# Kernel optimization log

Measured on AMD Instinct MI355X. Metric: run time of the kernel, lower is better.

## Reference

```python
import jax, jax.numpy as jnp
import numpy as np

N, H, E, G, OUT = 50000, 128, 600000, 256, 64
NUM_ITERS = 5
GAMMA = 0.1
EPS = 0.1
NEG_SLOPE = 0.01


def setup_inputs() -> dict:
    key = jax.random.key(0)
    ks = jax.random.split(key, 10)
    s = 1.0 / np.sqrt(H)
    x = jax.random.normal(ks[0], (N, H), dtype=jnp.float32)
    edge_index = jax.random.randint(ks[1], (2, E), 0, N, dtype=jnp.int64)
    batch = jnp.sort(jax.random.randint(ks[2], (N,), 0, G, dtype=jnp.int64))
    W = jax.random.normal(ks[3], (H, H), dtype=jnp.float32) * s
    bias = jax.random.normal(ks[4], (H,), dtype=jnp.float32) * s
    lin_w = jax.random.normal(ks[5], (H, H), dtype=jnp.float32) * s
    l1_w = jax.random.normal(ks[6], (3 * H // 2, 3 * H), dtype=jnp.float32) / np.sqrt(3 * H)
    l1_b = jax.random.normal(ks[7], (3 * H // 2,), dtype=jnp.float32) * 0.01
    l2_w = jax.random.normal(ks[8], (OUT, 3 * H // 2), dtype=jnp.float32) / np.sqrt(3 * H // 2)
    l2_b = jax.random.normal(ks[9], (OUT,), dtype=jnp.float32) * 0.01
    return {"x": x, "edge_index": edge_index, "batch": batch, "W": W, "bias": bias,
            "lin_w": lin_w, "l1_w": l1_w, "l1_b": l1_b, "l2_w": l2_w, "l2_b": l2_b}


def reference(x, edge_index, batch, W, bias, lin_w, l1_w, l1_b, l2_w, l2_b):
    n = x.shape[0]
    src, dst = edge_index[0], edge_index[1]
    # antisymmetric weight: W - W^T - gamma*I
    A = W - W.T - GAMMA * jnp.eye(W.shape[0], dtype=x.dtype)
    for _ in range(NUM_ITERS):
        neigh = x @ lin_w.T                                   # [N,H] linear (no bias)
        agg = jax.ops.segment_sum(neigh[src], dst, num_segments=n)  # gather-scatter add
        conv = x @ A.T + agg + bias
        x = x + EPS * jnp.tanh(conv)
    # triple global pooling per graph: add / max / mean
    add = jax.ops.segment_sum(x, batch, num_segments=G)
    mx = jax.ops.segment_max(x, batch, num_segments=G)
    cnt = jax.ops.segment_sum(jnp.ones((n,), dtype=x.dtype), batch, num_segments=G)
    safe_cnt = jnp.maximum(cnt, 1.0)[:, None]
    mean = add / safe_cnt
    mx = jnp.where(cnt[:, None] > 0, mx, 0.0)
    pooled = jnp.concatenate([add, mx, mean], axis=1)          # [G, 3H]
    h = jax.nn.leaky_relu(pooled @ l1_w.T + l1_b, NEG_SLOPE)
    out = jax.nn.leaky_relu(h @ l2_w.T + l2_b, NEG_SLOPE)
    return out
```

## Files before the change

kernel.cpp:

```cpp
#include <hip/hip_runtime.h>
#include <hip/hip_fp16.h>
#include <cmath>

#define H 128
#define GAMMA 0.1f
#define EPS 0.1f
#define NEG 0.01f
#define NGRAPH 256

typedef _Float16 half_t;
typedef _Float16 f16x8 __attribute__((ext_vector_type(8)));
typedef _Float16 f16x4 __attribute__((ext_vector_type(4)));
typedef _Float16 f16x2 __attribute__((ext_vector_type(2)));
typedef float f32x4 __attribute__((ext_vector_type(4)));

__device__ __forceinline__ float fast_tanh(float v) {
    float e = __builtin_amdgcn_exp2f(v * 2.8853900817779268f);
    float r = __builtin_amdgcn_rcpf(e + 1.0f);
    return 1.0f - 2.0f * r;
}

__global__ __launch_bounds__(256) void prep_cast_zero(
        const float* __restrict__ W, const float* __restrict__ lin_w,
        half_t* __restrict__ WtTf, const float* __restrict__ x,
        half_t* __restrict__ xh, int n4, int* __restrict__ deg, int N) {
    int stride = gridDim.x * 256;
    int tot = max(n4, max(32768, N));
    for (int i = blockIdx.x * 256 + threadIdx.x; i < tot; i += stride) {
        if (i < n4) {
            float4 v = *(const float4*)(x + (size_t)i * 4);
            half_t* o = xh + (size_t)i * 4;
            o[0] = (half_t)v.x; o[1] = (half_t)v.y; o[2] = (half_t)v.z; o[3] = (half_t)v.w;
        }
        if (i < 32768) {
            int t = i & 7;
            int lane = (i >> 3) & 63;
            int ct = (i >> 9) & 7;
            int s = i >> 12;
            int q = lane >> 4, m = lane & 15;
            int j = ct * 16 + m;
            int k = s * 32 + q * 8 + t;
            float v;
            if (k < H) v = W[j * H + k] - W[k * H + j] - (j == k ? GAMMA : 0.f);
            else       v = lin_w[j * H + (k - H)];
            WtTf[i] = (half_t)v;
        }
        if (i < N) deg[i] = 0;
    }
}

__global__ __launch_bounds__(256) void count_kernel(const int* __restrict__ dst,
                                                    int* __restrict__ deg, int E) {
    int stride = gridDim.x * 256;
    for (int e = blockIdx.x * 256 + threadIdx.x; e < E; e += stride)
        atomicAdd(&deg[dst[e]], 1);
}

#define SCHUNK 2048
__global__ __launch_bounds__(256) void scan_part(const int* __restrict__ deg,
                                                 int* __restrict__ partials, int N) {
    __shared__ int red[256];
    int t = threadIdx.x, b = blockIdx.x;
    int base = b * SCHUNK + t * 8;
    int s = 0;
#pragma unroll
    for (int i = 0; i < 8; ++i) { int idx = base + i; if (idx < N) s += deg[idx]; }
    red[t] = s;
    __syncthreads();
    for (int off = 128; off > 0; off >>= 1) {
        if (t < off) red[t] += red[t + off];
        __syncthreads();
    }
    if (t == 0) partials[b] = red[0];
}

__global__ void scan_mid(const int* __restrict__ partials, int* __restrict__ blkoff, int nblk) {
    int lane = threadIdx.x;
    int p = (lane < nblk) ? partials[lane] : 0;
    int v = p;
    for (int off = 1; off < 64; off <<= 1) {
        int u = __shfl_up(v, off);
        if (lane >= off) v += u;
    }
    if (lane < nblk) blkoff[lane] = v - p;
}

__global__ __launch_bounds__(256) void scan_final(const int* __restrict__ deg,
        const int* __restrict__ blkoff, int* __restrict__ row_start,
        int* __restrict__ cursor, int N, int E) {
    __shared__ int red[256];
    int t = threadIdx.x, b = blockIdx.x;
    int base = b * SCHUNK + t * 8;
    int v[8]; int s = 0;
#pragma unroll
    for (int i = 0; i < 8; ++i) { int idx = base + i; v[i] = (idx < N) ? deg[idx] : 0; s += v[i]; }
    red[t] = s;
    __syncthreads();
    for (int off = 1; off < 256; off <<= 1) {
        int u = (t >= off) ? red[t - off] : 0;
        __syncthreads();
        red[t] += u;
        __syncthreads();
    }
    int run = blkoff[b] + red[t] - s;
#pragma unroll
    for (int i = 0; i < 8; ++i) {
        int idx = base + i;
        if (idx < N) { row_start[idx] = run; cursor[idx] = run; run += v[i]; }
    }
    if (b == 0 && t == 0) row_start[N] = E;
}

__global__ __launch_bounds__(256) void fill_kernel(const int* __restrict__ src,
        const int* __restrict__ dst, int* __restrict__ cursor,
        int* __restrict__ csr_src, int E) {
    int stride = gridDim.x * 256;
    for (int e = blockIdx.x * 256 + threadIdx.x; e < E; e += stride) {
        int p = atomicAdd(&cursor[dst[e]], 1);
        csr_src[p] = src[e];
    }
}

__global__ __launch_bounds__(256) void gather_agg(const half_t* __restrict__ xh,
        const int* __restrict__ row_start, const int* __restrict__ csr_src,
        half_t* __restrict__ xaggh, int N) {
    int wid = __builtin_amdgcn_readfirstlane(blockIdx.x * 4 + (threadIdx.x >> 6));
    int nwaves = gridDim.x * 4;
    int lane = threadIdx.x & 63;
    for (int node = wid; node < N; node += nwaves) {
        int begin = row_start[node];
        int end   = row_start[node + 1];
        f16x2 accA = (f16x2){(half_t)0.f, (half_t)0.f};
        f16x2 accB = (f16x2){(half_t)0.f, (half_t)0.f};
        for (int base = begin; base < end; base += 64) {
            int cnt = min(64, end - base);
            int myidx = csr_src[base + min(lane, cnt - 1)];
            int j = 0;
            for (; j + 7 < cnt; j += 8) {
                int s0 = __builtin_amdgcn_readlane(myidx, j + 0);
                int s1 = __builtin_amdgcn_readlane(myidx, j + 1);
                int s2 = __builtin_amdgcn_readlane(myidx, j + 2);
                int s3 = __builtin_amdgcn_readlane(myidx, j + 3);
                int s4 = __builtin_amdgcn_readlane(myidx, j + 4);
                int s5 = __builtin_amdgcn_readlane(myidx, j + 5);
                int s6 = __builtin_amdgcn_readlane(myidx, j + 6);
                int s7 = __builtin_amdgcn_readlane(myidx, j + 7);
                f16x2 v0 = *(const f16x2*)(xh + (size_t)s0 * H + lane * 2);
                f16x2 v1 = *(const f16x2*)(xh + (size_t)s1 * H + lane * 2);
                f16x2 v2 = *(const f16x2*)(xh + (size_t)s2 * H + lane * 2);
                f16x2 v3 = *(const f16x2*)(xh + (size_t)s3 * H + lane * 2);
                f16x2 v4 = *(const f16x2*)(xh + (size_t)s4 * H + lane * 2);
                f16x2 v5 = *(const f16x2*)(xh + (size_t)s5 * H + lane * 2);
                f16x2 v6 = *(const f16x2*)(xh + (size_t)s6 * H + lane * 2);
                f16x2 v7 = *(const f16x2*)(xh + (size_t)s7 * H + lane * 2);
                accA += v0; accB += v1; accA += v2; accB += v3;
                accA += v4; accB += v5; accA += v6; accB += v7;
            }
            if (cnt - j >= 4) {
                int s0 = __builtin_amdgcn_readlane(myidx, j + 0);
                int s1 = __builtin_amdgcn_readlane(myidx, j + 1);
                int s2 = __builtin_amdgcn_readlane(myidx, j + 2);
                int s3 = __builtin_amdgcn_readlane(myidx, j + 3);
                f16x2 v0 = *(const f16x2*)(xh + (size_t)s0 * H + lane * 2);
                f16x2 v1 = *(const f16x2*)(xh + (size_t)s1 * H + lane * 2);
                f16x2 v2 = *(const f16x2*)(xh + (size_t)s2 * H + lane * 2);
                f16x2 v3 = *(const f16x2*)(xh + (size_t)s3 * H + lane * 2);
                accA += v0; accB += v1; accA += v2; accB += v3;
                j += 4;
            }
            int rem = cnt - j;
            if (rem > 0) {
                int s0 = __builtin_amdgcn_readlane(myidx, j);
                int s1 = __builtin_amdgcn_readlane(myidx, min(j + 1, cnt - 1));
                int s2 = __builtin_amdgcn_readlane(myidx, min(j + 2, cnt - 1));
                f16x2 v0 = *(const f16x2*)(xh + (size_t)s0 * H + lane * 2);
                f16x2 v1 = *(const f16x2*)(xh + (size_t)s1 * H + lane * 2);
                f16x2 v2 = *(const f16x2*)(xh + (size_t)s2 * H + lane * 2);
                accA += v0;
                if (rem > 1) accB += v1;
                if (rem > 2) accA += v2;
            }
        }
        f16x2 o = accA + accB;
        *(f16x2*)(xaggh + (size_t)node * H + lane * 2) = o;
    }
}

#define CROWS 128
__global__ __launch_bounds__(256) void conv_mfma(
        const half_t* __restrict__ xh, const half_t* __restrict__ xaggh,
        const half_t* __restrict__ WtTf, const float* __restrict__ bias,
        half_t* __restrict__ xhout, int N) {
    int tid = threadIdx.x;
    int wave = tid >> 6, lane = tid & 63;
    int q = lane >> 4, m = lane & 15;
    int n0 = blockIdx.x * CROWS + wave * 32;

    f32x4 acc[2][8];
#pragma unroll
    for (int rt = 0; rt < 2; ++rt)
#pragma unroll
        for (int ct = 0; ct < 8; ++ct) acc[rt][ct] = (f32x4){0.f, 0.f, 0.f, 0.f};

#pragma unroll
    for (int s = 0; s < 8; ++s) {
        f16x8 afrag[2];
#pragma unroll
        for (int rt = 0; rt < 2; ++rt) {
            int row = min(n0 + rt * 16 + m, N - 1);
            afrag[rt] = (s < 4)
                ? *(const f16x8*)(xh    + (size_t)row * H + s * 32 + q * 8)
                : *(const f16x8*)(xaggh + (size_t)row * H + (s - 4) * 32 + q * 8);
        }
#pragma unroll
        for (int ct = 0; ct < 8; ++ct) {
            f16x8 bfrag = *(const f16x8*)(WtTf + ((s * 8 + ct) * 64 + lane) * 8);
            acc[0][ct] = __builtin_amdgcn_mfma_f32_16x16x32_f16(afrag[0], bfrag, acc[0][ct], 0, 0, 0);
            acc[1][ct] = __builtin_amdgcn_mfma_f32_16x16x32_f16(afrag[1], bfrag, acc[1][ct], 0, 0, 0);
        }
    }

#pragma unroll
    for (int rt = 0; rt < 2; ++rt) {
#pragma unroll
        for (int r = 0; r < 4; ++r) {
            int row = n0 + rt * 16 + q * 4 + r;
            if (row < N) {
#pragma unroll
                for (int ct = 0; ct < 8; ++ct) {
                    int col = ct * 16 + m;
                    float c = acc[rt][ct][r] + bias[col];
                    float o = (float)xh[(size_t)row * H + col] + EPS * fast_tanh(c);
                    xhout[(size_t)row * H + col] = (half_t)o;
                }
            }
        }
    }
}

__global__ __launch_bounds__(1024) void pool_mlp(const half_t* __restrict__ x,
        const int* __restrict__ batch,
        const float* __restrict__ l1_w, const float* __restrict__ l1_b,
        const float* __restrict__ l2_w, const float* __restrict__ l2_b,
        float* __restrict__ out, int N) {
    __shared__ float ssum[8][128];
    __shared__ float smax[8][128];
    __shared__ __align__(16) float sp[384];
    __shared__ __align__(16) float sh[192];
    int g = blockIdx.x, t = threadIdx.x;
    int feat = t & 127, slot = t >> 7;
    int lo = 0, hi = N;
    while (lo < hi) { int mid = (lo + hi) >> 1; if (batch[mid] < g) lo = mid + 1; else hi = mid; }
    int start = lo;
    hi = N;
    while (lo < hi) { int mid = (lo + hi) >> 1; if (batch[mid] < g + 1) lo = mid + 1; else hi = mid; }
    int end = lo;
    float sum = 0.f, mx = -INFINITY;
    for (int n = start + slot; n < end; n += 8) {
        float v = (float)x[(size_t)n * H + feat];
        sum += v;
        mx = fmaxf(mx, v);
    }
    ssum[slot][feat] = sum;
    smax[slot][feat] = mx;
    __syncthreads();
    if (t < 128) {
        float s = 0.f, m = -INFINITY;
#pragma unroll
        for (int k = 0; k < 8; ++k) { s += ssum[k][t]; m = fmaxf(m, smax[k][t]); }
        int cnt = end - start;
        sp[t] = s;
        sp[128 + t] = (cnt > 0) ? m : 0.f;
        sp[256 + t] = s / (float)(cnt > 0 ? cnt : 1);
    }
    __syncthreads();
    if (t < 192) {
        float acc = l1_b[t];
        const float* wr = l1_w + (size_t)t * 384;
        for (int k = 0; k < 384; k += 4) {
            float4 w = *(const float4*)(wr + k);
            float4 p = *(const float4*)(sp + k);
            acc += w.x * p.x + w.y * p.y + w.z * p.z + w.w * p.w;
        }
        sh[t] = acc > 0.f ? acc : NEG * acc;
    }
    __syncthreads();
    if (t < 64) {
        float acc = l2_b[t];
        const float* wr = l2_w + (size_t)t * 192;
        for (int k = 0; k < 192; k += 4) {
            float4 w = *(const float4*)(wr + k);
            float4 p = *(const float4*)(sh + k);
            acc += w.x * p.x + w.y * p.y + w.z * p.z + w.w * p.w;
        }
        out[g * 64 + t] = acc > 0.f ? acc : NEG * acc;
    }
}

extern "C" void kernel_launch(void* const* d_in, const int* in_sizes, int n_in,
                              void* d_out, int out_size, void* d_ws, size_t ws_size,
                              hipStream_t stream) {
    const float* x0    = (const float*)d_in[0];
    const int*   edge  = (const int*)d_in[1];
    const int*   batch = (const int*)d_in[2];
    const float* W     = (const float*)d_in[3];
    const float* bias  = (const float*)d_in[4];
    const float* lin_w = (const float*)d_in[5];
    const float* l1_w  = (const float*)d_in[6];
    const float* l1_b  = (const float*)d_in[7];
    const float* l2_w  = (const float*)d_in[8];
    const float* l2_b  = (const float*)d_in[9];
    float* out = (float*)d_out;

    int N = in_sizes[0] / H;
    int E = in_sizes[1] / 2;
    const int* src = edge;
    const int* dst = edge + E;

    size_t nh = (size_t)N * H;
    half_t* xhA    = (half_t*)d_ws;
    half_t* xhB    = xhA + nh;
    half_t* xaggh  = xhB + nh;
    half_t* WtTf   = xaggh + nh;
    int* deg       = (int*)(WtTf + 32768);
    int* row_start = deg + N;
    int* cursor    = row_start + N + 1;
    int* csr_src   = cursor + N;
    int* partials  = csr_src + E;
    int* blkoff    = partials + 64;

    int n4 = (int)(nh / 4);
    prep_cast_zero<<<1024, 256, 0, stream>>>(W, lin_w, WtTf, x0, xhA, n4, deg, N);

    count_kernel<<<1024, 256, 0, stream>>>(dst, deg, E);
    int nblk = (N + SCHUNK - 1) / SCHUNK;
    scan_part<<<nblk, 256, 0, stream>>>(deg, partials, N);
    scan_mid<<<1, 64, 0, stream>>>(partials, blkoff, nblk);
    scan_final<<<nblk, 256, 0, stream>>>(deg, blkoff, row_start, cursor, N, E);
    fill_kernel<<<1024, 256, 0, stream>>>(src, dst, cursor, csr_src, E);

    const half_t* xcur_h = xhA;
    int nblocks = (N + CROWS - 1) / CROWS;
    for (int it = 0; it < 5; ++it) {
        gather_agg<<<2048, 256, 0, stream>>>(xcur_h, row_start, csr_src, xaggh, N);
        half_t* xnext_h = (it & 1) ? xhA : xhB;
        conv_mfma<<<nblocks, 256, 0, stream>>>(xcur_h, xaggh, WtTf, bias, xnext_h, N);
        xcur_h = xnext_h;
    }

    pool_mlp<<<NGRAPH, 1024, 0, stream>>>(xcur_h, batch, l1_w, l1_b, l2_w, l2_b, out, N);
}
```

Measured before the change: 381.2 us.

## Permute weight columns for vectorized conv epilogue and halve rows per wave

```diff
diff --git a/kernel.cpp b/kernel.cpp
--- a/kernel.cpp
+++ b/kernel.cpp
@@ -38,7 +38,7 @@
             int ct = (i >> 9) & 7;
             int s = i >> 12;
             int q = lane >> 4, m = lane & 15;
-            int j = ct * 16 + m;
+            int j = m * 8 + ct;
             int k = s * 32 + q * 8 + t;
             float v;
             if (k < H) v = W[j * H + k] - W[k * H + j] - (j == k ? GAMMA : 0.f);
@@ -186,7 +186,7 @@
     }
 }
 
-#define CROWS 128
+#define CROWS 64
 __global__ __launch_bounds__(256) void conv_mfma(
         const half_t* __restrict__ xh, const half_t* __restrict__ xaggh,
         const half_t* __restrict__ WtTf, const float* __restrict__ bias,
@@ -194,46 +194,40 @@
     int tid = threadIdx.x;
     int wave = tid >> 6, lane = tid & 63;
     int q = lane >> 4, m = lane & 15;
-    int n0 = blockIdx.x * CROWS + wave * 32;
-
-    f32x4 acc[2][8];
-#pragma unroll
-    for (int rt = 0; rt < 2; ++rt)
-#pragma unroll
-        for (int ct = 0; ct < 8; ++ct) acc[rt][ct] = (f32x4){0.f, 0.f, 0.f, 0.f};
-
+    int n0 = blockIdx.x * CROWS + wave * 16;
+
+    f32x4 acc[8];
+#pragma unroll
+    for (int ct = 0; ct < 8; ++ct) acc[ct] = (f32x4){0.f, 0.f, 0.f, 0.f};
+
+    int arow = min(n0 + m, N - 1);
 #pragma unroll
     for (int s = 0; s < 8; ++s) {
-        f16x8 afrag[2];
-#pragma unroll
-        for (int rt = 0; rt < 2; ++rt) {
-            int row = min(n0 + rt * 16 + m, N - 1);
-            afrag[rt] = (s < 4)
-                ? *(const f16x8*)(xh    + (size_t)row * H + s * 32 + q * 8)
-                : *(const f16x8*)(xaggh + (size_t)row * H + (s - 4) * 32 + q * 8);
-        }
+        f16x8 afrag = (s < 4)
+            ? *(const f16x8*)(xh    + (size_t)arow * H + s * 32 + q * 8)
+            : *(const f16x8*)(xaggh + (size_t)arow * H + (s - 4) * 32 + q * 8);
 #pragma unroll
         for (int ct = 0; ct < 8; ++ct) {
             f16x8 bfrag = *(const f16x8*)(WtTf + ((s * 8 + ct) * 64 + lane) * 8);
-            acc[0][ct] = __builtin_amdgcn_mfma_f32_16x16x32_f16(afrag[0], bfrag, acc[0][ct], 0, 0, 0);
-            acc[1][ct] = __builtin_amdgcn_mfma_f32_16x16x32_f16(afrag[1], bfrag, acc[1][ct], 0, 0, 0);
-        }
-    }
-
-#pragma unroll
-    for (int rt = 0; rt < 2; ++rt) {
-#pragma unroll
-        for (int r = 0; r < 4; ++r) {
-            int row = n0 + rt * 16 + q * 4 + r;
-            if (row < N) {
-#pragma unroll
-                for (int ct = 0; ct < 8; ++ct) {
-                    int col = ct * 16 + m;
-                    float c = acc[rt][ct][r] + bias[col];
-                    float o = (float)xh[(size_t)row * H + col] + EPS * fast_tanh(c);
-                    xhout[(size_t)row * H + col] = (half_t)o;
-                }
+            acc[ct] = __builtin_amdgcn_mfma_f32_16x16x32_f16(afrag, bfrag, acc[ct], 0, 0, 0);
+        }
+    }
+
+    float4 b0 = *(const float4*)(bias + m * 8);
+    float4 b1 = *(const float4*)(bias + m * 8 + 4);
+    float bb[8] = {b0.x, b0.y, b0.z, b0.w, b1.x, b1.y, b1.z, b1.w};
+#pragma unroll
+    for (int r = 0; r < 4; ++r) {
+        int row = n0 + q * 4 + r;
+        if (row < N) {
+            f16x8 xr = *(const f16x8*)(xh + (size_t)row * H + m * 8);
+            f16x8 o;
+#pragma unroll
+            for (int ct = 0; ct < 8; ++ct) {
+                float c = acc[ct][r] + bb[ct];
+                o[ct] = (half_t)((float)xr[ct] + EPS * fast_tanh(c));
             }
+            *(f16x8*)(xhout + (size_t)row * H + m * 8) = o;
         }
     }
 }
```

Result: faster. 372.7 us (-2.2%).
